# Kernel tuning notes

Measured on AMD Instinct MI355X. Metric: run time of the kernel, lower is better.

Reference implementation:

```python
import jax, jax.numpy as jnp
import numpy as np

B, S, N, C, OUT = 16, 1024, 4096, 768, 256


def setup_inputs() -> dict:
    key = jax.random.key(0)
    k0, k1, k2, k3, k4 = jax.random.split(key, 5)
    seed_xyz = jax.random.normal(k0, (B, S, 3), jnp.float32)   # normalized seed coords
    p_last = jax.random.normal(k1, (B, N, 3), jnp.float32)     # lift3d last-stage coords
    f_last = jax.random.normal(k2, (B, C, N), jnp.float32)     # lift3d last-stage features (channel-first)
    W = jax.random.normal(k3, (OUT, C), jnp.float32) * 0.02    # Conv1d(C, 256, kernel_size=1) weight
    b = jax.random.normal(k4, (OUT,), jnp.float32) * 0.02      # Conv1d bias
    return {"seed_xyz": seed_xyz, "p_last": p_last, "f_last": f_last, "W": W, "b": b}


def reference(seed_xyz, p_last, f_last, W, b):
    # Squared pairwise distances [B,S,N] (argmin invariant to sqrt)
    d2 = (jnp.sum(seed_xyz * seed_xyz, axis=-1, keepdims=True)          # [B,S,1]
          - 2.0 * jnp.einsum('bsd,bnd->bsn', seed_xyz, p_last)          # [B,S,N]
          + jnp.sum(p_last * p_last, axis=-1)[:, None, :])              # [B,1,N]
    idx = jnp.argmin(d2, axis=-1)                                       # [B,S]
    # Gather nearest-neighbor features: [B,C,N] -> [B,C,S]
    gathered = jnp.take_along_axis(f_last, idx[:, None, :], axis=2)
    # 1x1 Conv1d projector: [B,C,S] x [OUT,C] -> [B,OUT,S]
    seed_features = jnp.einsum('bcs,oc->bos', gathered, W) + b[None, :, None]
    return seed_features
```

## Files before the change

### kernel.cpp

```cpp
#include <hip/hip_runtime.h>
#include <stdint.h>

#define B_   16
#define S_   1024
#define N_   4096
#define C_   768
#define OUT_ 256

typedef short bf16x8 __attribute__((ext_vector_type(8)));
typedef float f32x4  __attribute__((ext_vector_type(4)));

#define GLOBAL_AS __attribute__((address_space(1)))
#define LDS_AS    __attribute__((address_space(3)))

__device__ __forceinline__ unsigned short f2bf(float f) {
    unsigned int u = __float_as_uint(f);
    u += 0x7fffu + ((u >> 16) & 1u);
    return (unsigned short)(u >> 16);
}

__device__ __forceinline__ void gl_lds16(const void* gsrc, void* ldst) {
    __builtin_amdgcn_global_load_lds((const GLOBAL_AS void*)gsrc,
                                     (LDS_AS void*)ldst, 16, 0, 0);
}

__global__ __launch_bounds__(256) void k_wconv(const float* __restrict__ W,
                                               unsigned short* __restrict__ Wb) {
    int i = blockIdx.x * 256 + threadIdx.x;
    Wb[i] = f2bf(W[i]);
}

__global__ __launch_bounds__(256) void k_argmin(const float* __restrict__ seed,
                                                const float* __restrict__ pl,
                                                int* __restrict__ idx_out) {
    const int t    = threadIdx.x;
    const int lane = t & 63;
    const int w    = t >> 6;
    const int gw   = blockIdx.x * 4 + w;
    const int b    = gw >> 8;
    const int s0   = (gw & 255) * 4;

    float sx[4], sy[4], sz[4], s2[4], best[4];
    int   bidx[4];
#pragma unroll
    for (int j = 0; j < 4; ++j) {
        const float* sp = seed + (size_t)(b * S_ + s0 + j) * 3;
        sx[j] = sp[0]; sy[j] = sp[1]; sz[j] = sp[2];
        s2[j] = __fadd_rn(__fadd_rn(__fmul_rn(sx[j], sx[j]),
                                    __fmul_rn(sy[j], sy[j])),
                          __fmul_rn(sz[j], sz[j]));
        best[j] = 3.4e38f;
        bidx[j] = 0;
    }
    const float* pb = pl + (size_t)b * N_ * 3;

    for (int k = 0; k < N_ / 64; ++k) {
        const int   n  = k * 64 + lane;
        const float px = pb[n * 3 + 0];
        const float py = pb[n * 3 + 1];
        const float pz = pb[n * 3 + 2];
        const float p2 = __fadd_rn(__fadd_rn(__fmul_rn(px, px),
                                             __fmul_rn(py, py)),
                                   __fmul_rn(pz, pz));
#pragma unroll
        for (int j = 0; j < 4; ++j) {
            float dot = __fadd_rn(__fadd_rn(__fmul_rn(sx[j], px),
                                            __fmul_rn(sy[j], py)),
                                  __fmul_rn(sz[j], pz));
            float d2  = __fadd_rn(__fsub_rn(s2[j], __fmul_rn(2.0f, dot)), p2);
            if (d2 < best[j]) { best[j] = d2; bidx[j] = n; }
        }
    }

#pragma unroll
    for (int j = 0; j < 4; ++j) {
#pragma unroll
        for (int off = 32; off >= 1; off >>= 1) {
            float ob = __shfl_xor(best[j], off, 64);
            int   oi = __shfl_xor(bidx[j], off, 64);
            bool take = (ob < best[j]) || (ob == best[j] && oi < bidx[j]);
            if (take) { best[j] = ob; bidx[j] = oi; }
        }
        if (lane == 0) idx_out[b * S_ + s0 + j] = bidx[j];
    }
}

#define CT 8
__global__ __launch_bounds__(256) void k_gather(const float* __restrict__ f,
                                                const int* __restrict__ idx,
                                                unsigned short* __restrict__ gt) {
    __shared__ float buf[2][N_];
    const int t  = threadIdx.x;
    const int b  = blockIdx.x / 96;
    const int ct = blockIdx.x % 96;
    const int c0 = ct * CT;

    int idxv[4];
#pragma unroll
    for (int j = 0; j < 4; ++j) idxv[j] = idx[b * S_ + t + 256 * j];

    const float* fb = f + ((size_t)b * C_ + c0) * N_;

#pragma unroll
    for (int k = 0; k < 4; ++k)
        gl_lds16(fb + t * 4 + k * 1024, &buf[0][t * 4 + k * 1024]);

    unsigned short og[4][CT] __attribute__((aligned(16)));

#pragma unroll
    for (int j = 0; j < CT; ++j) {
        __syncthreads();
        if (j + 1 < CT) {
            const float* row = fb + (size_t)(j + 1) * N_;
            float* dst = &buf[(j + 1) & 1][0];
#pragma unroll
            for (int k = 0; k < 4; ++k)
                gl_lds16(row + t * 4 + k * 1024, dst + t * 4 + k * 1024);
        }
        const float* src = &buf[j & 1][0];
#pragma unroll
        for (int si = 0; si < 4; ++si)
            og[si][j] = f2bf(src[idxv[si]]);
    }

    const size_t ob = (size_t)b * S_ * C_ + c0;
#pragma unroll
    for (int si = 0; si < 4; ++si) {
        int s = t + si * 256;
        *(uint4*)(gt + ob + (size_t)s * C_) = *(const uint4*)og[si];
    }
}

__global__ __launch_bounds__(256) void k_gemm(const unsigned short* __restrict__ Wb,
                                              const unsigned short* __restrict__ gt,
                                              const float* __restrict__ bias,
                                              float* __restrict__ out) {
    __shared__ unsigned short ldsA[128 * 32];
    __shared__ unsigned short ldsB[128 * 32];
    const int t    = threadIdx.x;
    const int bid  = blockIdx.x;
    const int b    = bid >> 4;
    const int mt   = (bid >> 3) & 1;
    const int nt   = bid & 7;
    const int m0   = mt * 128;
    const int n0   = nt * 128;
    const int lane = t & 63;
    const int w    = t >> 6;
    const int wm   = w & 1, wn = w >> 1;
    const int quad = lane >> 4, l16 = lane & 15;

    f32x4 acc[4][4];
#pragma unroll
    for (int i = 0; i < 4; ++i)
#pragma unroll
        for (int j = 0; j < 4; ++j) acc[i][j] = (f32x4){0.f, 0.f, 0.f, 0.f};

    const int rowS = t >> 2;
    const int kkS  = (t & 3) * 8;
    const unsigned short* aSrc0 = Wb + (size_t)(m0 + rowS) * C_ + kkS;
    const unsigned short* aSrc1 = Wb + (size_t)(m0 + 64 + rowS) * C_ + kkS;
    const unsigned short* bBase = gt + (size_t)b * S_ * C_;
    const unsigned short* bSrc0 = bBase + (size_t)(n0 + rowS) * C_ + kkS;
    const unsigned short* bSrc1 = bBase + (size_t)(n0 + 64 + rowS) * C_ + kkS;
    unsigned short* la = ldsA + t * 8;
    unsigned short* lb = ldsB + t * 8;

    for (int kt = 0; kt < C_ / 32; ++kt) {
        const int k0 = kt * 32;
        gl_lds16(aSrc0 + k0, la);
        gl_lds16(aSrc1 + k0, la + 2048);
        gl_lds16(bSrc0 + k0, lb);
        gl_lds16(bSrc1 + k0, lb + 2048);
        __syncthreads();

        bf16x8 aF[4], bF[4];
#pragma unroll
        for (int mi = 0; mi < 4; ++mi)
            aF[mi] = *(const bf16x8*)(ldsA + ((wm * 64 + mi * 16 + l16) * 32 + quad * 8));
#pragma unroll
        for (int ni = 0; ni < 4; ++ni)
            bF[ni] = *(const bf16x8*)(ldsB + ((wn * 64 + ni * 16 + l16) * 32 + quad * 8));
#pragma unroll
        for (int mi = 0; mi < 4; ++mi)
#pragma unroll
            for (int ni = 0; ni < 4; ++ni)
                acc[mi][ni] = __builtin_amdgcn_mfma_f32_16x16x32_bf16(
                    aF[mi], bF[ni], acc[mi][ni], 0, 0, 0);
        __syncthreads();
    }

    float* obase = out + (size_t)b * OUT_ * S_;
#pragma unroll
    for (int mi = 0; mi < 4; ++mi) {
#pragma unroll
        for (int r = 0; r < 4; ++r) {
            const int o  = m0 + wm * 64 + mi * 16 + quad * 4 + r;
            const float bo = bias[o];
            float* orow = obase + (size_t)o * S_;
#pragma unroll
            for (int ni = 0; ni < 4; ++ni) {
                const int s = n0 + wn * 64 + ni * 16 + l16;
                orow[s] = acc[mi][ni][r] + bo;
            }
        }
    }
}

extern "C" void kernel_launch(void* const* d_in, const int* in_sizes, int n_in,
                              void* d_out, int out_size, void* d_ws, size_t ws_size,
                              hipStream_t stream) {
    const float* seed = (const float*)d_in[0];
    const float* pl   = (const float*)d_in[1];
    const float* f    = (const float*)d_in[2];
    const float* W    = (const float*)d_in[3];
    const float* bias = (const float*)d_in[4];
    float* out = (float*)d_out;

    int* idx            = (int*)d_ws;
    unsigned short* Wb  = (unsigned short*)((char*)d_ws + 65536);
    unsigned short* gt  = (unsigned short*)((char*)d_ws + 524288);

    k_wconv <<<768,  256, 0, stream>>>(W, Wb);
    k_argmin<<<1024, 256, 0, stream>>>(seed, pl, idx);
    k_gather<<<1536, 256, 0, stream>>>(f, idx, gt);
    k_gemm  <<<256,  256, 0, stream>>>(Wb, gt, bias, out);
}
```

Before: 359.1 us.

## Project all points before gathering instead of gathering then projecting

Reorders the pipeline so the 1x1 conv projection is applied to every point's features first (reading fp32 features directly into the GEMM), storing a bf16 projected table, then gathers nearest-neighbor rows and adds bias. This removes the separate gather pass and its strided LDS lookups, at the cost of four times more matrix FLOPs and an extra bf16 rounding of the projected output.

```diff
diff --git a/kernel.cpp b/kernel.cpp
--- a/kernel.cpp
+++ b/kernel.cpp
@@ -8,6 +8,7 @@
 #define OUT_ 256
 
 typedef short bf16x8 __attribute__((ext_vector_type(8)));
+typedef short bf16x4 __attribute__((ext_vector_type(4)));
 typedef float f32x4  __attribute__((ext_vector_type(4)));
 
 #define GLOBAL_AS __attribute__((address_space(1)))
@@ -85,124 +86,119 @@
     }
 }
 
-#define CT 8
-__global__ __launch_bounds__(256) void k_gather(const float* __restrict__ f,
-                                                const int* __restrict__ idx,
-                                                unsigned short* __restrict__ gt) {
-    __shared__ float buf[2][N_];
-    const int t  = threadIdx.x;
-    const int b  = blockIdx.x / 96;
-    const int ct = blockIdx.x % 96;
-    const int c0 = ct * CT;
-
-    int idxv[4];
-#pragma unroll
-    for (int j = 0; j < 4; ++j) idxv[j] = idx[b * S_ + t + 256 * j];
-
-    const float* fb = f + ((size_t)b * C_ + c0) * N_;
-
-#pragma unroll
-    for (int k = 0; k < 4; ++k)
-        gl_lds16(fb + t * 4 + k * 1024, &buf[0][t * 4 + k * 1024]);
-
-    unsigned short og[4][CT] __attribute__((aligned(16)));
-
-#pragma unroll
-    for (int j = 0; j < CT; ++j) {
-        __syncthreads();
-        if (j + 1 < CT) {
-            const float* row = fb + (size_t)(j + 1) * N_;
-            float* dst = &buf[(j + 1) & 1][0];
-#pragma unroll
-            for (int k = 0; k < 4; ++k)
-                gl_lds16(row + t * 4 + k * 1024, dst + t * 4 + k * 1024);
-        }
-        const float* src = &buf[j & 1][0];
-#pragma unroll
-        for (int si = 0; si < 4; ++si)
-            og[si][j] = f2bf(src[idxv[si]]);
-    }
-
-    const size_t ob = (size_t)b * S_ * C_ + c0;
-#pragma unroll
-    for (int si = 0; si < 4; ++si) {
-        int s = t + si * 256;
-        *(uint4*)(gt + ob + (size_t)s * C_) = *(const uint4*)og[si];
-    }
-}
-
-__global__ __launch_bounds__(256) void k_gemm(const unsigned short* __restrict__ Wb,
-                                              const unsigned short* __restrict__ gt,
-                                              const float* __restrict__ bias,
-                                              float* __restrict__ out) {
-    __shared__ unsigned short ldsA[128 * 32];
-    __shared__ unsigned short ldsB[128 * 32];
+__global__ __launch_bounds__(256, 2) void k_pgemm(const float* __restrict__ f,
+                                                  const unsigned short* __restrict__ Wb,
+                                                  unsigned short* __restrict__ P) {
+    __shared__ unsigned short ldsF[128 * 36];
+    __shared__ unsigned short ldsW[256 * 32];
     const int t    = threadIdx.x;
-    const int bid  = blockIdx.x;
-    const int b    = bid >> 4;
-    const int mt   = (bid >> 3) & 1;
-    const int nt   = bid & 7;
-    const int m0   = mt * 128;
+    const int b    = blockIdx.x >> 5;
+    const int nt   = blockIdx.x & 31;
     const int n0   = nt * 128;
     const int lane = t & 63;
     const int w    = t >> 6;
-    const int wm   = w & 1, wn = w >> 1;
+    const int wm   = w & 1;
+    const int wo   = w >> 1;
     const int quad = lane >> 4, l16 = lane & 15;
 
-    f32x4 acc[4][4];
+    f32x4 acc[4][8];
 #pragma unroll
     for (int i = 0; i < 4; ++i)
 #pragma unroll
-        for (int j = 0; j < 4; ++j) acc[i][j] = (f32x4){0.f, 0.f, 0.f, 0.f};
-
-    const int rowS = t >> 2;
-    const int kkS  = (t & 3) * 8;
-    const unsigned short* aSrc0 = Wb + (size_t)(m0 + rowS) * C_ + kkS;
-    const unsigned short* aSrc1 = Wb + (size_t)(m0 + 64 + rowS) * C_ + kkS;
-    const unsigned short* bBase = gt + (size_t)b * S_ * C_;
-    const unsigned short* bSrc0 = bBase + (size_t)(n0 + rowS) * C_ + kkS;
-    const unsigned short* bSrc1 = bBase + (size_t)(n0 + 64 + rowS) * C_ + kkS;
-    unsigned short* la = ldsA + t * 8;
-    unsigned short* lb = ldsB + t * 8;
+        for (int j = 0; j < 8; ++j) acc[i][j] = (f32x4){0.f, 0.f, 0.f, 0.f};
+
+    const int cb = t >> 5;
+    const int nb = t & 31;
+    const float* fB = f + (size_t)b * C_ * N_ + n0 + nb * 4;
+    const unsigned short* wSrc = Wb + (size_t)(t >> 2) * C_ + (t & 3) * 8;
 
     for (int kt = 0; kt < C_ / 32; ++kt) {
         const int k0 = kt * 32;
-        gl_lds16(aSrc0 + k0, la);
-        gl_lds16(aSrc1 + k0, la + 2048);
-        gl_lds16(bSrc0 + k0, lb);
-        gl_lds16(bSrc1 + k0, lb + 2048);
+#pragma unroll
+        for (int i = 0; i < 4; ++i)
+            gl_lds16(wSrc + (size_t)i * 64 * C_ + k0, ldsW + i * 2048 + t * 8);
+        f32x4 v[4];
+#pragma unroll
+        for (int j = 0; j < 4; ++j)
+            v[j] = *(const f32x4*)(fB + (size_t)(k0 + cb * 4 + j) * N_);
+#pragma unroll
+        for (int i = 0; i < 4; ++i) {
+            bf16x4 pk = {(short)f2bf(v[0][i]), (short)f2bf(v[1][i]),
+                         (short)f2bf(v[2][i]), (short)f2bf(v[3][i])};
+            *(bf16x4*)(ldsF + (nb * 4 + i) * 36 + cb * 4) = pk;
+        }
         __syncthreads();
 
-        bf16x8 aF[4], bF[4];
+        bf16x8 aF[4], bF[8];
+#pragma unroll
+        for (int mi = 0; mi < 4; ++mi) {
+            const unsigned short* p = ldsF + (wm * 64 + mi * 16 + l16) * 36 + quad * 8;
+            bf16x4 lo = *(const bf16x4*)p;
+            bf16x4 hi = *(const bf16x4*)(p + 4);
+            aF[mi] = __builtin_shufflevector(lo, hi, 0, 1, 2, 3, 4, 5, 6, 7);
+        }
+#pragma unroll
+        for (int oi = 0; oi < 8; ++oi)
+            bF[oi] = *(const bf16x8*)(ldsW + (wo * 128 + oi * 16 + l16) * 32 + quad * 8);
 #pragma unroll
         for (int mi = 0; mi < 4; ++mi)
-            aF[mi] = *(const bf16x8*)(ldsA + ((wm * 64 + mi * 16 + l16) * 32 + quad * 8));
-#pragma unroll
-        for (int ni = 0; ni < 4; ++ni)
-            bF[ni] = *(const bf16x8*)(ldsB + ((wn * 64 + ni * 16 + l16) * 32 + quad * 8));
-#pragma unroll
-        for (int mi = 0; mi < 4; ++mi)
-#pragma unroll
-            for (int ni = 0; ni < 4; ++ni)
-                acc[mi][ni] = __builtin_amdgcn_mfma_f32_16x16x32_bf16(
-                    aF[mi], bF[ni], acc[mi][ni], 0, 0, 0);
+#pragma unroll
+            for (int oi = 0; oi < 8; ++oi)
+                acc[mi][oi] = __builtin_amdgcn_mfma_f32_16x16x32_bf16(
+                    aF[mi], bF[oi], acc[mi][oi], 0, 0, 0);
         __syncthreads();
     }
 
-    float* obase = out + (size_t)b * OUT_ * S_;
+    unsigned short* Pb = P + ((size_t)b * N_ + n0) * OUT_;
 #pragma unroll
     for (int mi = 0; mi < 4; ++mi) {
 #pragma unroll
         for (int r = 0; r < 4; ++r) {
-            const int o  = m0 + wm * 64 + mi * 16 + quad * 4 + r;
-            const float bo = bias[o];
-            float* orow = obase + (size_t)o * S_;
-#pragma unroll
-            for (int ni = 0; ni < 4; ++ni) {
-                const int s = n0 + wn * 64 + ni * 16 + l16;
-                orow[s] = acc[mi][ni][r] + bo;
+            const int n = wm * 64 + mi * 16 + quad * 4 + r;
+            unsigned short* row = Pb + (size_t)n * OUT_;
+#pragma unroll
+            for (int oi = 0; oi < 8; ++oi) {
+                const int o = wo * 128 + oi * 16 + l16;
+                row[o] = f2bf(acc[mi][oi][r]);
             }
         }
+    }
+}
+
+__global__ __launch_bounds__(256) void k_out(const unsigned short* __restrict__ P,
+                                             const int* __restrict__ idx,
+                                             const float* __restrict__ bias,
+                                             float* __restrict__ out) {
+    __shared__ unsigned short tl[64 * 260];
+    const int t  = threadIdx.x;
+    const int b  = blockIdx.x >> 4;
+    const int st = blockIdx.x & 15;
+    const int s0 = st * 64;
+    const unsigned short* Pb = P + (size_t)b * N_ * OUT_;
+
+#pragma unroll
+    for (int i = 0; i < 8; ++i) {
+        const int g = i * 256 + t;
+        const int s = g >> 5;
+        const int p = g & 31;
+        const int n = idx[b * S_ + s0 + s];
+        const unsigned short* src = Pb + (size_t)n * OUT_ + p * 8;
+        uint2 u0 = *(const uint2*)src;
+        uint2 u1 = *(const uint2*)(src + 4);
+        *(uint2*)(tl + s * 260 + p * 8)     = u0;
+        *(uint2*)(tl + s * 260 + p * 8 + 4) = u1;
+    }
+    __syncthreads();
+
+    const int lane = t & 63;
+    const int w    = t >> 6;
+    float* ob = out + (size_t)b * OUT_ * S_ + s0;
+#pragma unroll 4
+    for (int oo = 0; oo < 64; ++oo) {
+        const int o = w * 64 + oo;
+        const unsigned short u = tl[lane * 260 + o];
+        const float val = __uint_as_float(((unsigned int)u) << 16) + bias[o];
+        ob[(size_t)o * S_ + lane] = val;
     }
 }
 
@@ -218,10 +214,10 @@
 
     int* idx            = (int*)d_ws;
     unsigned short* Wb  = (unsigned short*)((char*)d_ws + 65536);
-    unsigned short* gt  = (unsigned short*)((char*)d_ws + 524288);
+    unsigned short* P   = (unsigned short*)((char*)d_ws + 524288);
 
     k_wconv <<<768,  256, 0, stream>>>(W, Wb);
     k_argmin<<<1024, 256, 0, stream>>>(seed, pl, idx);
-    k_gather<<<1536, 256, 0, stream>>>(f, idx, gt);
-    k_gemm  <<<256,  256, 0, stream>>>(Wb, gt, bias, out);
-}
+    k_pgemm <<<512,  256, 0, stream>>>(f, Wb, P);
+    k_out   <<<256,  256, 0, stream>>>(P, idx, bias, out);
+}
```

Measured after the change: 320.9 us. 10.6% less time.
